# Kernel optimization log

Measured on AMD Instinct MI355X. Metric: run time of the kernel, lower is better.

## Reference

```python
import jax, jax.numpy as jnp
import numpy as np
import math

B, TQ, TK, C, H, DFF = 4, 1024, 1024, 1024, 16, 4096
DK = C // H
EPS = 1e-12


def _mha(x_q, x_kv, wq, bq, wk, bk, wv, bv, wo, bo, mask):
    Bq, Tq, Cq = x_q.shape
    Tk = x_kv.shape[1]
    q = (x_q @ wq + bq).reshape(Bq, Tq, H, DK).transpose(0, 2, 1, 3)  # [B,H,Tq,dk]
    k = (x_kv @ wk + bk).reshape(Bq, Tk, H, DK).transpose(0, 2, 1, 3)
    v = (x_kv @ wv + bv).reshape(Bq, Tk, H, DK).transpose(0, 2, 1, 3)
    scores = jnp.einsum('bhqd,bhkd->bhqk', q, k) * (1.0 / math.sqrt(DK))
    if mask is not None:
        scores = jnp.where(mask, scores, jnp.asarray(-1e9, scores.dtype))
    attn = jax.nn.softmax(scores, axis=-1)
    o = jnp.einsum('bhqk,bhkd->bhqd', attn, v).transpose(0, 2, 1, 3).reshape(Bq, Tq, Cq)
    return o @ wo + bo


def _ln(x, g, b):
    mu = jnp.mean(x, axis=-1, keepdims=True)
    var = jnp.mean(jnp.square(x - mu), axis=-1, keepdims=True)
    return (x - mu) * jax.lax.rsqrt(var + EPS) * g + b


def setup_inputs() -> dict:
    key = jax.random.key(0)
    ks = iter(jax.random.split(key, 32))
    s = 0.02
    inp = {}
    inp['src'] = jax.random.normal(next(ks), (B, TK, C), jnp.float32)
    inp['dst'] = jax.random.normal(next(ks), (B, TQ, C), jnp.float32)
    inp['src_mask'] = jnp.ones((B, 1, 1, TK), dtype=bool)  # key-padding mask (all valid)
    inp['dst_mask'] = jnp.tril(jnp.ones((TQ, TQ), dtype=bool))[None, None]  # causal
    for p in ['sa', 'ca']:
        for n in ['wq', 'wk', 'wv', 'wo']:
            inp[f'{p}_{n}'] = jax.random.normal(next(ks), (C, C), jnp.float32) * s
        for n in ['bq', 'bk', 'bv', 'bo']:
            inp[f'{p}_{n}'] = jnp.zeros((C,), jnp.float32)
    inp['ffn_w1'] = jax.random.normal(next(ks), (C, DFF), jnp.float32) * s
    inp['ffn_b1'] = jnp.zeros((DFF,), jnp.float32)
    inp['ffn_w2'] = jax.random.normal(next(ks), (DFF, C), jnp.float32) * s
    inp['ffn_b2'] = jnp.zeros((C,), jnp.float32)
    for i in ['1', '2', '3']:
        inp[f'ln{i}_g'] = jnp.ones((C,), jnp.float32)
        inp[f'ln{i}_b'] = jnp.zeros((C,), jnp.float32)
    return inp


def reference(src, dst, src_mask, dst_mask,
              sa_wq, sa_wk, sa_wv, sa_wo, sa_bq, sa_bk, sa_bv, sa_bo,
              ca_wq, ca_wk, ca_wv, ca_wo, ca_bq, ca_bk, ca_bv, ca_bo,
              ffn_w1, ffn_b1, ffn_w2, ffn_b2,
              ln1_g, ln1_b, ln2_g, ln2_b, ln3_g, ln3_b):
    # post-LN decoder layer, eval mode (dropout is identity)
    sa = _mha(dst, dst, sa_wq, sa_bq, sa_wk, sa_bk, sa_wv, sa_bv, sa_wo, sa_bo, dst_mask)
    y = _ln(dst + sa, ln1_g, ln1_b)
    ca = _mha(y, src, ca_wq, ca_bq, ca_wk, ca_bk, ca_wv, ca_bv, ca_wo, ca_bo, src_mask)
    y = _ln(y + ca, ln2_g, ln2_b)
    ff = jax.nn.gelu(y @ ffn_w1 + ffn_b1, approximate=False) @ ffn_w2 + ffn_b2
    return _ln(y + ff, ln3_g, ln3_b)
```

## Files before the change

### kernel.cpp

```cpp
#include <hip/hip_runtime.h>
#include <math.h>


typedef __attribute__((ext_vector_type(4))) float f32x4;
typedef __attribute__((ext_vector_type(8))) __bf16 bf16x8;
typedef __attribute__((ext_vector_type(8))) short short8;

#define DEV __device__ __forceinline__

DEV short f2bfs(float f) {
    unsigned u = __builtin_bit_cast(unsigned, f);
    unsigned r = (u + 0x7FFFu + ((u >> 16) & 1u)) >> 16;
    return (short)r;
}

DEV f32x4 mfma16(bf16x8 a, bf16x8 b, f32x4 c) {
    return __builtin_amdgcn_mfma_f32_16x16x32_bf16(a, b, c, 0, 0, 0);
}

DEV void gload_lds16(const void* g, void* l) {
    __builtin_amdgcn_global_load_lds((const __attribute__((address_space(1))) void*)g,
                                     (__attribute__((address_space(3))) void*)l, 16, 0, 0);
}

__global__ __launch_bounds__(256) void wtrans(const float* __restrict__ Win,
                                              short* __restrict__ Wout,
                                              int Kd, int Nd) {
    __shared__ float Tt[64][65];
    const int tx = threadIdx.x & 15, ty = threadIdx.x >> 4;
    const int k0 = blockIdx.y * 64, n0 = blockIdx.x * 64;
#pragma unroll
    for (int rr = 0; rr < 4; ++rr) {
        int k = ty + rr * 16;
        float4 v = *(const float4*)&Win[(size_t)(k0 + k) * Nd + n0 + tx * 4];
        Tt[k][tx * 4 + 0] = v.x; Tt[k][tx * 4 + 1] = v.y;
        Tt[k][tx * 4 + 2] = v.z; Tt[k][tx * 4 + 3] = v.w;
    }
    __syncthreads();
#pragma unroll
    for (int rr = 0; rr < 4; ++rr) {
        int n = ty + rr * 16;
        short4 o;
        o.x = f2bfs(Tt[tx * 4 + 0][n]);
        o.y = f2bfs(Tt[tx * 4 + 1][n]);
        o.z = f2bfs(Tt[tx * 4 + 2][n]);
        o.w = f2bfs(Tt[tx * 4 + 3][n]);
        *(short4*)&Wout[(size_t)(n0 + n) * Kd + k0 + tx * 4] = o;
    }
}

struct WPtrs { const float* p[8]; };

__global__ __launch_bounds__(256) void wtrans8(WPtrs wp, short* __restrict__ out) {
    const float* __restrict__ Win = wp.p[blockIdx.z];
    short* __restrict__ Wout = out + (size_t)blockIdx.z * (1024 * 1024);
    __shared__ float Tt[64][65];
    const int tx = threadIdx.x & 15, ty = threadIdx.x >> 4;
    const int k0 = blockIdx.y * 64, n0 = blockIdx.x * 64;
#pragma unroll
    for (int rr = 0; rr < 4; ++rr) {
        int k = ty + rr * 16;
        float4 v = *(const float4*)&Win[(size_t)(k0 + k) * 1024 + n0 + tx * 4];
        Tt[k][tx * 4 + 0] = v.x; Tt[k][tx * 4 + 1] = v.y;
        Tt[k][tx * 4 + 2] = v.z; Tt[k][tx * 4 + 3] = v.w;
    }
    __syncthreads();
#pragma unroll
    for (int rr = 0; rr < 4; ++rr) {
        int n = ty + rr * 16;
        short4 o;
        o.x = f2bfs(Tt[tx * 4 + 0][n]);
        o.y = f2bfs(Tt[tx * 4 + 1][n]);
        o.z = f2bfs(Tt[tx * 4 + 2][n]);
        o.w = f2bfs(Tt[tx * 4 + 3][n]);
        *(short4*)&Wout[(size_t)(n0 + n) * 1024 + k0 + tx * 4] = o;
    }
}

__global__ __launch_bounds__(256) void conv_bf16(const float* __restrict__ X,
                                                 short* __restrict__ Y, int n8) {
    int i = blockIdx.x * 256 + threadIdx.x;
    if (i < n8) {
        float4 a = ((const float4*)X)[i * 2];
        float4 b = ((const float4*)X)[i * 2 + 1];
        short8 o;
        o[0] = f2bfs(a.x); o[1] = f2bfs(a.y); o[2] = f2bfs(a.z); o[3] = f2bfs(a.w);
        o[4] = f2bfs(b.x); o[5] = f2bfs(b.y); o[6] = f2bfs(b.z); o[7] = f2bfs(b.w);
        ((short8*)Y)[i] = o;
    }
}

template <int BM, int BN, int BK, int EPI, int SWZ>
__global__ __launch_bounds__(256, (BM == 64 && BN == 64) ? 4 : 1)
void gemm_bt(const short* __restrict__ A,
             const short* __restrict__ BT,
             const float* __restrict__ b0,
             const float* __restrict__ b1,
             const float* __restrict__ b2,
             void* __restrict__ o0,
             void* __restrict__ o1,
             void* __restrict__ o2,
             int M, int N, int K, int Ks) {
    constexpr int IM = BM / 32, JN = BN / 32;
    constexpr int KH = BK / 32;
    constexpr int AL = (BM * 64) / 4096;
    constexpr int BL = (BN * 64) / 4096;
    __shared__ __align__(16) short As[2][BM * BK];
    __shared__ __align__(16) short Bs[2][BN * BK];
    const int tid = threadIdx.x, lane = tid & 63, w = tid >> 6;

    int bx, by, bz;
    if (SWZ == 1) {
        int gx = gridDim.x, gy = gridDim.y;
        int G = gx * gy * gridDim.z;
        int fid = blockIdx.x + gx * (blockIdx.y + gy * blockIdx.z);
        int nf = (fid & 7) * (G >> 3) + (fid >> 3);
        bx = nf % gx;
        int t = nf / gx;
        by = t % gy;
        bz = t / gy;
    } else {
        bx = blockIdx.x; by = blockIdx.y; bz = blockIdx.z;
    }

    const int m0 = by * BM, n0 = bx * BN;
    const int kz = bz * K;
    const int wm = (w & 1) * (BM / 2), wn = (w >> 1) * (BN / 2);
    const int rl = lane & 15, rg = lane >> 4;
    f32x4 acc[IM][JN] = {};
    const char* Ab = (const char*)A;
    const char* Bb = (const char*)BT;
    const int nk = K / BK;

    auto stage = [&](int kt, int buf) {
#pragma unroll
        for (int h = 0; h < KH; ++h) {
#pragma unroll
            for (int r = 0; r < AL; ++r) {
                int lo = (tid + r * 256) * 16;
                int row = lo >> 6, cp = (lo >> 4) & 3, c = (cp - (row >> 1)) & 3;
                gload_lds16(Ab + ((size_t)(m0 + row) * Ks + kz + kt * BK + h * 32 + c * 8) * 2,
                            (char*)As[buf] + h * (BM * 64) + lo);
            }
#pragma unroll
            for (int r = 0; r < BL; ++r) {
                int lo = (tid + r * 256) * 16;
                int row = lo >> 6, cp = (lo >> 4) & 3, c = (cp - (row >> 1)) & 3;
                gload_lds16(Bb + ((size_t)(n0 + row) * Ks + kz + kt * BK + h * 32 + c * 8) * 2,
                            (char*)Bs[buf] + h * (BN * 64) + lo);
            }
        }
    };

    stage(0, 0);
    for (int kt = 0; kt < nk; ++kt) {
        const int buf = kt & 1;
        __syncthreads();
        if (kt + 1 < nk) stage(kt + 1, buf ^ 1);
        bf16x8 af[KH][IM], bfr[KH][JN];
#pragma unroll
        for (int h = 0; h < KH; ++h) {
#pragma unroll
            for (int i = 0; i < IM; i++) {
                int row = wm + i * 16 + rl;
                af[h][i] = *(const bf16x8*)(As[buf] + h * (BM * 32) + row * 32 +
                                            ((rg + (row >> 1)) & 3) * 8);
            }
#pragma unroll
            for (int j = 0; j < JN; j++) {
                int row = wn + j * 16 + rl;
                bfr[h][j] = *(const bf16x8*)(Bs[buf] + h * (BN * 32) + row * 32 +
                                             ((rg + (row >> 1)) & 3) * 8);
            }
        }
#pragma unroll
        for (int h = 0; h < KH; ++h)
#pragma unroll
            for (int i = 0; i < IM; i++)
#pragma unroll
                for (int j = 0; j < JN; j++)
                    acc[i][j] = mfma16(af[h][i], bfr[h][j], acc[i][j]);
    }

    float* o0z = (float*)o0 + (size_t)bz * M * N;
#pragma unroll
    for (int i = 0; i < IM; i++) {
        int gm0 = m0 + wm + i * 16 + rg * 4;
#pragma unroll
        for (int j = 0; j < JN; j++) {
            int gn = n0 + wn + j * 16 + rl;
            if (EPI == 0) {
                float bv = bz == 0 ? b0[gn] : 0.0f;
#pragma unroll
                for (int r = 0; r < 4; r++)
                    o0z[(size_t)(gm0 + r) * N + gn] = acc[i][j][r] + bv;
            } else if (EPI == 2) {
                float bv = b0[gn];
#pragma unroll
                for (int r = 0; r < 4; r++) {
                    float x = acc[i][j][r] + bv;
                    float z = 1.59576912f * x + 0.07135481f * x * x * x;
                    float g = x / (1.0f + __expf(-z));
                    ((short*)o0)[(size_t)(gm0 + r) * N + gn] = f2bfs(g);
                }
            } else {
                int seg = gn >> 10, n1 = gn & 1023, h = n1 >> 6, d = n1 & 63;
                int b = gm0 >> 10, t0 = gm0 & 1023;
                bool isV = (EPI == 1) ? (seg == 2) : (seg == 1);
                const float* bp = (EPI == 1) ? (seg == 0 ? b0 : (seg == 1 ? b1 : b2))
                                             : (seg == 0 ? b0 : b1);
                float bv = bp[n1];
                float qs = (EPI == 1 && seg == 0) ? 0.125f : 1.0f;
                if (!isV) {
                    short* hp = (short*)((EPI == 1) ? (seg == 0 ? o0 : o1) : o0);
                    size_t base = ((size_t)(b * 16 + h) * 1024 + t0) * 64 + d;
#pragma unroll
                    for (int r = 0; r < 4; r++)
                        hp[base + (size_t)r * 64] = f2bfs((acc[i][j][r] + bv) * qs);
                } else {
                    short* vp = (short*)((EPI == 1) ? o2 : o1);
                    short4 pk;
                    pk.x = f2bfs(acc[i][j][0] + bv);
                    pk.y = f2bfs(acc[i][j][1] + bv);
                    pk.z = f2bfs(acc[i][j][2] + bv);
                    pk.w = f2bfs(acc[i][j][3] + bv);
                    *(short4*)(vp + ((size_t)(b * 16 + h) * 64 + d) * 1024 + t0) = pk;
                }
            }
        }
    }
}

template <bool CAUSAL>
__global__ __launch_bounds__(256, 3) void attn4(const short* __restrict__ Qh,
                                                const short* __restrict__ Kh,
                                                const short* __restrict__ VTh,
                                                short* __restrict__ Out, int TKn) {
    __shared__ __align__(16) short Ks[2][64 * 64];
    __shared__ __align__(16) short Vts[2][64 * 64];
    __shared__ __align__(16) short Ps[4][16 * 72 + 8];
    const int tid = threadIdx.x, lane = tid & 63, w = tid >> 6;
    const int rl = lane & 15, rg = lane >> 4;
    const int bh = blockIdx.y, b = bh >> 4, h = bh & 15;
    const int qb = CAUSAL ? (gridDim.x - 1 - blockIdx.x) : blockIdx.x;
    const int q0 = qb * 64;
    const short* Qp = Qh + (size_t)bh * 1024 * 64;
    const char* Kp = (const char*)(Kh + (size_t)bh * (size_t)TKn * 64);
    const char* Vp = (const char*)(VTh + (size_t)bh * (size_t)TKn * 64);

    const int qrow = q0 + w * 16 + rl;
    const bf16x8 qf0 = *(const bf16x8*)(Qp + (size_t)qrow * 64 + rg * 8);
    const bf16x8 qf1 = *(const bf16x8*)(Qp + (size_t)qrow * 64 + 32 + rg * 8);

    bf16x8 onesf;
#pragma unroll
    for (int i = 0; i < 8; ++i) onesf[i] = (__bf16)1.0f;

    f32x4 o[4] = {};
    f32x4 lacc = {};

    short* Pw = &Ps[w][0];
    const int nkt = CAUSAL ? qb + 1 : (TKn >> 6);

    auto stage = [&](int kt, int buf) {
#pragma unroll
        for (int r = 0; r < 2; ++r) {
            int lo = (w * 2 + r) * 1024 + lane * 16;
            int row = lo >> 7, cp = (lo >> 4) & 7, c = (cp - row) & 7;
            gload_lds16(Kp + ((size_t)(kt * 64 + row) * 64 + c * 8) * 2,
                        (char*)Ks[buf] + lo);
            gload_lds16(Vp + ((size_t)row * TKn + kt * 64 + c * 8) * 2,
                        (char*)Vts[buf] + lo);
        }
    };

    stage(0, 0);
    for (int kt = 0; kt < nkt; ++kt) {
        const int buf = kt & 1;
        __syncthreads();
        if (kt + 1 < nkt) stage(kt + 1, buf ^ 1);

        const short* KsB = Ks[buf];
        f32x4 s[4];
#pragma unroll
        for (int ch = 0; ch < 4; ++ch) {
            int row = ch * 16 + rl;
            bf16x8 k0 = *(const bf16x8*)(KsB + row * 64 + ((rg + row) & 7) * 8);
            bf16x8 k1 = *(const bf16x8*)(KsB + row * 64 + ((rg + 4 + row) & 7) * 8);
            f32x4 z = {};
            z = mfma16(k0, qf0, z);
            z = mfma16(k1, qf1, z);
            s[ch] = z;
        }
        const bool domask = CAUSAL && (kt == nkt - 1);
#pragma unroll
        for (int ch = 0; ch < 4; ++ch) {
            float p[4];
#pragma unroll
            for (int r = 0; r < 4; ++r) {
                float e = __expf(s[ch][r]);
                if (domask) {
                    int key = kt * 64 + ch * 16 + rg * 4 + r;
                    if (key > qrow) e = 0.0f;
                }
                p[r] = e;
            }
            unsigned d0 = (__builtin_bit_cast(unsigned, p[1]) & 0xFFFF0000u) |
                          (__builtin_bit_cast(unsigned, p[0]) >> 16);
            unsigned d1 = (__builtin_bit_cast(unsigned, p[3]) & 0xFFFF0000u) |
                          (__builtin_bit_cast(unsigned, p[2]) >> 16);
            uint2 dv; dv.x = d0; dv.y = d1;
            *(uint2*)(Pw + rl * 72 + ch * 16 + rg * 4) = dv;
        }
        bf16x8 pa0 = *(const bf16x8*)(Pw + rl * 72 + rg * 8);
        bf16x8 pa1 = *(const bf16x8*)(Pw + rl * 72 + 32 + rg * 8);
        lacc = mfma16(pa0, onesf, lacc);
        lacc = mfma16(pa1, onesf, lacc);
        const short* VsB = Vts[buf];
#pragma unroll
        for (int j = 0; j < 4; ++j) {
            int row = j * 16 + rl;
            bf16x8 v0 = *(const bf16x8*)(VsB + row * 64 + ((rg + row) & 7) * 8);
            bf16x8 v1 = *(const bf16x8*)(VsB + row * 64 + ((rg + 4 + row) & 7) * 8);
            o[j] = mfma16(pa0, v0, o[j]);
            o[j] = mfma16(pa1, v1, o[j]);
        }
    }

    float inv[4];
#pragma unroll
    for (int r = 0; r < 4; r++) inv[r] = 1.0f / lacc[r];
#pragma unroll
    for (int j = 0; j < 4; j++) {
#pragma unroll
        for (int r = 0; r < 4; r++) {
            int row = q0 + w * 16 + rg * 4 + r;
            int col = h * 64 + j * 16 + rl;
            Out[((size_t)b * 1024 + row) * 1024 + col] = f2bfs(o[j][r] * inv[r]);
        }
    }
}

__global__ __launch_bounds__(256) void ln_fused(const float* __restrict__ X,
                                                const float* __restrict__ R,
                                                const float* __restrict__ R2,
                                                const float* __restrict__ gam,
                                                const float* __restrict__ bet,
                                                float* __restrict__ Yf,
                                                short* __restrict__ Yb) {
    const int row = blockIdx.x, tid = threadIdx.x;
    const int lane = tid & 63, w = tid >> 6;
    float4 xv = ((const float4*)(X + (size_t)row * 1024))[tid];
    float4 rv = ((const float4*)(R + (size_t)row * 1024))[tid];
    float v0 = xv.x + rv.x, v1 = xv.y + rv.y, v2 = xv.z + rv.z, v3 = xv.w + rv.w;
    if (R2) {
        float4 r2 = ((const float4*)(R2 + (size_t)row * 1024))[tid];
        v0 += r2.x; v1 += r2.y; v2 += r2.z; v3 += r2.w;
    }
    float s = v0 + v1 + v2 + v3;
    float ss = v0 * v0 + v1 * v1 + v2 * v2 + v3 * v3;
#pragma unroll
    for (int off = 1; off < 64; off <<= 1) {
        s += __shfl_xor(s, off);
        ss += __shfl_xor(ss, off);
    }
    __shared__ float sred[4], ssred[4];
    if (lane == 0) { sred[w] = s; ssred[w] = ss; }
    __syncthreads();
    s = sred[0] + sred[1] + sred[2] + sred[3];
    ss = ssred[0] + ssred[1] + ssred[2] + ssred[3];
    float mu = s * (1.0f / 1024.0f);
    float var = ss * (1.0f / 1024.0f) - mu * mu;
    float rsq = rsqrtf(var + 1e-12f);
    float4 gv = ((const float4*)gam)[tid];
    float4 bv = ((const float4*)bet)[tid];
    float y0 = (v0 - mu) * rsq * gv.x + bv.x;
    float y1 = (v1 - mu) * rsq * gv.y + bv.y;
    float y2 = (v2 - mu) * rsq * gv.z + bv.z;
    float y3 = (v3 - mu) * rsq * gv.w + bv.w;
    float4 yo = {y0, y1, y2, y3};
    ((float4*)(Yf + (size_t)row * 1024))[tid] = yo;
    if (Yb) {
        short4 ob;
        ob.x = f2bfs(y0); ob.y = f2bfs(y1); ob.z = f2bfs(y2); ob.w = f2bfs(y3);
        ((short4*)(Yb + (size_t)row * 1024))[tid] = ob;
    }
}

extern "C" void kernel_launch(void* const* d_in, const int* in_sizes, int n_in,
                              void* d_out, int out_size, void* d_ws, size_t ws_size,
                              hipStream_t stream) {
    const float* src = (const float*)d_in[0];
    const float* dst = (const float*)d_in[1];
    const float* sa_wq = (const float*)d_in[4];
    const float* sa_wk = (const float*)d_in[5];
    const float* sa_wv = (const float*)d_in[6];
    const float* sa_wo = (const float*)d_in[7];
    const float* sa_bq = (const float*)d_in[8];
    const float* sa_bk = (const float*)d_in[9];
    const float* sa_bv = (const float*)d_in[10];
    const float* sa_bo = (const float*)d_in[11];
    const float* ca_wq = (const float*)d_in[12];
    const float* ca_wk = (const float*)d_in[13];
    const float* ca_wv = (const float*)d_in[14];
    const float* ca_wo = (const float*)d_in[15];
    const float* ca_bq = (const float*)d_in[16];
    const float* ca_bk = (const float*)d_in[17];
    const float* ca_bv = (const float*)d_in[18];
    const float* ca_bo = (const float*)d_in[19];
    const float* ffn_w1 = (const float*)d_in[20];
    const float* ffn_b1 = (const float*)d_in[21];
    const float* ffn_w2 = (const float*)d_in[22];
    const float* ffn_b2 = (const float*)d_in[23];
    const float* ln1g = (const float*)d_in[24];
    const float* ln1b = (const float*)d_in[25];
    const float* ln2g = (const float*)d_in[26];
    const float* ln2b = (const float*)d_in[27];
    const float* ln3g = (const float*)d_in[28];
    const float* ln3b = (const float*)d_in[29];

    char* ws = (char*)d_ws;
    size_t off = 0;
    auto alloc = [&](size_t n) { size_t o = off; off = (off + n + 255) & ~(size_t)255; return o; };

    const size_t szW = (size_t)1024 * 1024 * 2;
    short* wT = (short*)(ws + alloc(8 * szW));
    short* w1T = (short*)(ws + alloc((size_t)4096 * 1024 * 2));
    short* w2T = (short*)(ws + alloc((size_t)1024 * 4096 * 2));
    const size_t szAct2 = (size_t)4096 * 1024 * 2;
    const size_t szAct4 = (size_t)4096 * 1024 * 4;
    short* dstb = (short*)(ws + alloc(szAct2));
    short* srcb = (short*)(ws + alloc(szAct2));
    short* Qh = (short*)(ws + alloc(szAct2));
    short* Kh = (short*)(ws + alloc(szAct2));
    short* VTh = (short*)(ws + alloc(szAct2));
    short* attnb = (short*)(ws + alloc(szAct2));
    float* tmp = (float*)(ws + alloc(szAct4));
    float* y1f = (float*)(ws + alloc(szAct4));
    short* y1b = (short*)(ws + alloc(szAct2));
    float* y2f = (float*)(ws + alloc(szAct4));
    short* y2b = (short*)(ws + alloc(szAct2));
    short* ffnh = (short*)(ws + alloc((size_t)4096 * 4096 * 2));

    short* sa_wqkvT = wT;
    short* sa_woT = wT + 3 * (size_t)1048576;
    short* ca_wqT = wT + 4 * (size_t)1048576;
    short* ca_wkvT = wT + 5 * (size_t)1048576;
    short* ca_woT = wT + 7 * (size_t)1048576;

    dim3 blk(256);

    WPtrs wp = {{sa_wq, sa_wk, sa_wv, sa_wo, ca_wq, ca_wk, ca_wv, ca_wo}};
    wtrans8<<<dim3(16, 16, 8), blk, 0, stream>>>(wp, wT);
    wtrans<<<dim3(64, 16), blk, 0, stream>>>(ffn_w1, w1T, 1024, 4096);
    wtrans<<<dim3(16, 64), blk, 0, stream>>>(ffn_w2, w2T, 4096, 1024);
    conv_bf16<<<2048, blk, 0, stream>>>(dst, dstb, 524288);
    conv_bf16<<<2048, blk, 0, stream>>>(src, srcb, 524288);

    gemm_bt<128, 128, 32, 1, 0><<<dim3(24, 32), blk, 0, stream>>>(
        dstb, sa_wqkvT, sa_bq, sa_bk, sa_bv, Qh, Kh, VTh, 4096, 3072, 1024, 1024);
    attn4<true><<<dim3(16, 64), blk, 0, stream>>>(Qh, Kh, VTh, attnb, 1024);
    gemm_bt<64, 64, 64, 0, 1><<<dim3(16, 64), blk, 0, stream>>>(
        attnb, sa_woT, sa_bo, nullptr, nullptr, tmp, nullptr, nullptr, 4096, 1024, 1024, 1024);
    ln_fused<<<4096, blk, 0, stream>>>(dst, tmp, nullptr, ln1g, ln1b, y1f, y1b);

    gemm_bt<64, 64, 64, 1, 1><<<dim3(16, 64), blk, 0, stream>>>(
        y1b, ca_wqT, ca_bq, nullptr, nullptr, Qh, nullptr, nullptr, 4096, 1024, 1024, 1024);
    gemm_bt<128, 128, 32, 3, 0><<<dim3(16, 32), blk, 0, stream>>>(
        srcb, ca_wkvT, ca_bk, ca_bv, nullptr, Kh, VTh, nullptr, 4096, 2048, 1024, 1024);
    attn4<false><<<dim3(16, 64), blk, 0, stream>>>(Qh, Kh, VTh, attnb, 1024);
    gemm_bt<64, 64, 64, 0, 1><<<dim3(16, 64), blk, 0, stream>>>(
        attnb, ca_woT, ca_bo, nullptr, nullptr, tmp, nullptr, nullptr, 4096, 1024, 1024, 1024);
    ln_fused<<<4096, blk, 0, stream>>>(y1f, tmp, nullptr, ln2g, ln2b, y2f, y2b);

    gemm_bt<128, 128, 32, 2, 0><<<dim3(32, 32), blk, 0, stream>>>(
        y2b, w1T, ffn_b1, nullptr, nullptr, ffnh, nullptr, nullptr, 4096, 4096, 1024, 1024);
    gemm_bt<64, 64, 64, 0, 1><<<dim3(16, 64), blk, 0, stream>>>(
        ffnh, w2T, ffn_b2, nullptr, nullptr, tmp, nullptr, nullptr, 4096, 1024, 4096, 4096);
    ln_fused<<<4096, blk, 0, stream>>>(y2f, tmp, nullptr, ln3g, ln3b, (float*)d_out, nullptr);

    (void)in_sizes; (void)n_in; (void)out_size; (void)ws_size;
}
```

Before: 514.8 us.

## Merge self-attn QKV and cross-attn KV projections into one GEMM launch

Combines the self-attention QKV projection and the cross-attention K/V projection (which depends only on src) into a single gemm launch with 40 column tiles, routing blocks with bx>=24 to the src/ca weights and dedicated caKh/caVTh buffers. It also merges the two fp32-to-bf16 conversion kernels into one launch. The aim is to cut launch count and fill the GPU better with a larger grid (1280 blocks instead of 768 and 512 separately). The cost is two extra workspace buffers and a branchier epilogue.

```diff
diff --git a/kernel.cpp b/kernel.cpp
--- a/kernel.cpp
+++ b/kernel.cpp
@@ -1,6 +1,5 @@
 #include <hip/hip_runtime.h>
 #include <math.h>
-
 
 typedef __attribute__((ext_vector_type(4))) float f32x4;
 typedef __attribute__((ext_vector_type(8))) __bf16 bf16x8;
@@ -22,6 +21,15 @@
     __builtin_amdgcn_global_load_lds((const __attribute__((address_space(1))) void*)g,
                                      (__attribute__((address_space(3))) void*)l, 16, 0, 0);
 }
+
+struct QKV5P {
+    const short* A2;
+    const short* B2;
+    const float* b3;
+    const float* b4;
+    void* o3;
+    void* o4;
+};
 
 __global__ __launch_bounds__(256) void wtrans(const float* __restrict__ Win,
                                               short* __restrict__ Wout,
@@ -77,16 +85,21 @@
     }
 }
 
-__global__ __launch_bounds__(256) void conv_bf16(const float* __restrict__ X,
-                                                 short* __restrict__ Y, int n8) {
+__global__ __launch_bounds__(256) void conv_bf16_2(const float* __restrict__ Xa,
+                                                   short* __restrict__ Ya,
+                                                   const float* __restrict__ Xb,
+                                                   short* __restrict__ Yb, int n8) {
     int i = blockIdx.x * 256 + threadIdx.x;
-    if (i < n8) {
-        float4 a = ((const float4*)X)[i * 2];
-        float4 b = ((const float4*)X)[i * 2 + 1];
+    const float* X; short* Y; int j;
+    if (i < n8) { X = Xa; Y = Ya; j = i; }
+    else        { X = Xb; Y = Yb; j = i - n8; }
+    if (j < n8) {
+        float4 a = ((const float4*)X)[j * 2];
+        float4 b = ((const float4*)X)[j * 2 + 1];
         short8 o;
         o[0] = f2bfs(a.x); o[1] = f2bfs(a.y); o[2] = f2bfs(a.z); o[3] = f2bfs(a.w);
         o[4] = f2bfs(b.x); o[5] = f2bfs(b.y); o[6] = f2bfs(b.z); o[7] = f2bfs(b.w);
-        ((short8*)Y)[i] = o;
+        ((short8*)Y)[j] = o;
     }
 }
 
@@ -100,7 +113,7 @@
              void* __restrict__ o0,
              void* __restrict__ o1,
              void* __restrict__ o2,
-             int M, int N, int K, int Ks) {
+             int M, int N, int K, int Ks, QKV5P ex) {
     constexpr int IM = BM / 32, JN = BN / 32;
     constexpr int KH = BK / 32;
     constexpr int AL = (BM * 64) / 4096;
@@ -123,13 +136,23 @@
         bx = blockIdx.x; by = blockIdx.y; bz = blockIdx.z;
     }
 
-    const int m0 = by * BM, n0 = bx * BN;
+    const int m0 = by * BM;
+    int n0 = bx * BN;
+    const char* Ab = (const char*)A;
+    const char* Bb = (const char*)BT;
+    bool isCA = false;
+    if constexpr (EPI == 4) {
+        if (bx >= 24) {
+            isCA = true;
+            n0 = (bx - 24) * BN;
+            Ab = (const char*)ex.A2;
+            Bb = (const char*)ex.B2;
+        }
+    }
     const int kz = bz * K;
     const int wm = (w & 1) * (BM / 2), wn = (w >> 1) * (BN / 2);
     const int rl = lane & 15, rg = lane >> 4;
     f32x4 acc[IM][JN] = {};
-    const char* Ab = (const char*)A;
-    const char* Bb = (const char*)BT;
     const int nk = K / BK;
 
     auto stage = [&](int kt, int buf) {
@@ -202,6 +225,49 @@
                     float z = 1.59576912f * x + 0.07135481f * x * x * x;
                     float g = x / (1.0f + __expf(-z));
                     ((short*)o0)[(size_t)(gm0 + r) * N + gn] = f2bfs(g);
+                }
+            } else if (EPI == 4) {
+                int seg = gn >> 10, n1 = gn & 1023, h = n1 >> 6, d = n1 & 63;
+                int b = gm0 >> 10, t0 = gm0 & 1023;
+                if (!isCA) {
+                    bool isV = seg == 2;
+                    const float* bp = seg == 0 ? b0 : (seg == 1 ? b1 : b2);
+                    float bv = bp[n1];
+                    float qs = seg == 0 ? 0.125f : 1.0f;
+                    if (!isV) {
+                        short* hp = (short*)(seg == 0 ? o0 : o1);
+                        size_t base = ((size_t)(b * 16 + h) * 1024 + t0) * 64 + d;
+#pragma unroll
+                        for (int r = 0; r < 4; r++)
+                            hp[base + (size_t)r * 64] = f2bfs((acc[i][j][r] + bv) * qs);
+                    } else {
+                        short* vp = (short*)o2;
+                        short4 pk;
+                        pk.x = f2bfs(acc[i][j][0] + bv);
+                        pk.y = f2bfs(acc[i][j][1] + bv);
+                        pk.z = f2bfs(acc[i][j][2] + bv);
+                        pk.w = f2bfs(acc[i][j][3] + bv);
+                        *(short4*)(vp + ((size_t)(b * 16 + h) * 64 + d) * 1024 + t0) = pk;
+                    }
+                } else {
+                    bool isV = seg == 1;
+                    const float* bp = seg == 0 ? ex.b3 : ex.b4;
+                    float bv = bp[n1];
+                    if (!isV) {
+                        short* hp = (short*)ex.o3;
+                        size_t base = ((size_t)(b * 16 + h) * 1024 + t0) * 64 + d;
+#pragma unroll
+                        for (int r = 0; r < 4; r++)
+                            hp[base + (size_t)r * 64] = f2bfs(acc[i][j][r] + bv);
+                    } else {
+                        short* vp = (short*)ex.o4;
+                        short4 pk;
+                        pk.x = f2bfs(acc[i][j][0] + bv);
+                        pk.y = f2bfs(acc[i][j][1] + bv);
+                        pk.z = f2bfs(acc[i][j][2] + bv);
+                        pk.w = f2bfs(acc[i][j][3] + bv);
+                        *(short4*)(vp + ((size_t)(b * 16 + h) * 64 + d) * 1024 + t0) = pk;
+                    }
                 }
             } else {
                 int seg = gn >> 10, n1 = gn & 1023, h = n1 >> 6, d = n1 & 63;
@@ -434,6 +500,8 @@
     short* Qh = (short*)(ws + alloc(szAct2));
     short* Kh = (short*)(ws + alloc(szAct2));
     short* VTh = (short*)(ws + alloc(szAct2));
+    short* caKh = (short*)(ws + alloc(szAct2));
+    short* caVTh = (short*)(ws + alloc(szAct2));
     short* attnb = (short*)(ws + alloc(szAct2));
     float* tmp = (float*)(ws + alloc(szAct4));
     float* y1f = (float*)(ws + alloc(szAct4));
@@ -449,34 +517,33 @@
     short* ca_woT = wT + 7 * (size_t)1048576;
 
     dim3 blk(256);
+    QKV5P noex = {};
 
     WPtrs wp = {{sa_wq, sa_wk, sa_wv, sa_wo, ca_wq, ca_wk, ca_wv, ca_wo}};
     wtrans8<<<dim3(16, 16, 8), blk, 0, stream>>>(wp, wT);
     wtrans<<<dim3(64, 16), blk, 0, stream>>>(ffn_w1, w1T, 1024, 4096);
     wtrans<<<dim3(16, 64), blk, 0, stream>>>(ffn_w2, w2T, 4096, 1024);
-    conv_bf16<<<2048, blk, 0, stream>>>(dst, dstb, 524288);
-    conv_bf16<<<2048, blk, 0, stream>>>(src, srcb, 524288);
-
-    gemm_bt<128, 128, 32, 1, 0><<<dim3(24, 32), blk, 0, stream>>>(
-        dstb, sa_wqkvT, sa_bq, sa_bk, sa_bv, Qh, Kh, VTh, 4096, 3072, 1024, 1024);
+    conv_bf16_2<<<4096, blk, 0, stream>>>(dst, dstb, src, srcb, 524288);
+
+    QKV5P qx = {srcb, ca_wkvT, ca_bk, ca_bv, caKh, caVTh};
+    gemm_bt<128, 128, 32, 4, 0><<<dim3(40, 32), blk, 0, stream>>>(
+        dstb, sa_wqkvT, sa_bq, sa_bk, sa_bv, Qh, Kh, VTh, 4096, 3072, 1024, 1024, qx);
     attn4<true><<<dim3(16, 64), blk, 0, stream>>>(Qh, Kh, VTh, attnb, 1024);
     gemm_bt<64, 64, 64, 0, 1><<<dim3(16, 64), blk, 0, stream>>>(
-        attnb, sa_woT, sa_bo, nullptr, nullptr, tmp, nullptr, nullptr, 4096, 1024, 1024, 1024);
+        attnb, sa_woT, sa_bo, nullptr, nullptr, tmp, nullptr, nullptr, 4096, 1024, 1024, 1024, noex);
     ln_fused<<<4096, blk, 0, stream>>>(dst, tmp, nullptr, ln1g, ln1b, y1f, y1b);
 
     gemm_bt<64, 64, 64, 1, 1><<<dim3(16, 64), blk, 0, stream>>>(
-        y1b, ca_wqT, ca_bq, nullptr, nullptr, Qh, nullptr, nullptr, 4096, 1024, 1024, 1024);
-    gemm_bt<128, 128, 32, 3, 0><<<dim3(16, 32), blk, 0, stream>>>(
-        srcb, ca_wkvT, ca_bk, ca_bv, nullptr, Kh, VTh, nullptr, 4096, 2048, 1024, 1024);
-    attn4<false><<<dim3(16, 64), blk, 0, stream>>>(Qh, Kh, VTh, attnb, 1024);
+        y1b, ca_wqT, ca_bq, nullptr, nullptr, Qh, nullptr, nullptr, 4096, 1024, 1024, 1024, noex);
+    attn4<false><<<dim3(16, 64), blk, 0, stream>>>(Qh, caKh, caVTh, attnb, 1024);
     gemm_bt<64, 64, 64, 0, 1><<<dim3(16, 64), blk, 0, stream>>>(
-        attnb, ca_woT, ca_bo, nullptr, nullptr, tmp, nullptr, nullptr, 4096, 1024, 1024, 1024);
+        attnb, ca_woT, ca_bo, nullptr, nullptr, tmp, nullptr, nullptr, 4096, 1024, 1024, 1024, noex);
     ln_fused<<<4096, blk, 0, stream>>>(y1f, tmp, nullptr, ln2g, ln2b, y2f, y2b);
 
     gemm_bt<128, 128, 32, 2, 0><<<dim3(32, 32), blk, 0, stream>>>(
-        y2b, w1T, ffn_b1, nullptr, nullptr, ffnh, nullptr, nullptr, 4096, 4096, 1024, 1024);
+        y2b, w1T, ffn_b1, nullptr, nullptr, ffnh, nullptr, nullptr, 4096, 4096, 1024, 1024, noex);
     gemm_bt<64, 64, 64, 0, 1><<<dim3(16, 64), blk, 0, stream>>>(
-        ffnh, w2T, ffn_b2, nullptr, nullptr, tmp, nullptr, nullptr, 4096, 1024, 4096, 4096);
+        ffnh, w2T, ffn_b2, nullptr, nullptr, tmp, nullptr, nullptr, 4096, 1024, 4096, 4096, noex);
     ln_fused<<<4096, blk, 0, stream>>>(y2f, tmp, nullptr, ln3g, ln3b, (float*)d_out, nullptr);
 
     (void)in_sizes; (void)n_in; (void)out_size; (void)ws_size;
```

Measured after the change: 517.3 us. Within noise of the previous version (+0.5%).
